# Kernel optimization log

Measured on AMD Instinct MI355X. Metric: run time of the kernel, lower is better.

## Reference

```python
import jax, jax.numpy as jnp
import numpy as np
import math

B, SQ, SKV, D, H, DFF = 8, 256, 1024, 1024, 16, 4096
DK = D // H
EPS = 1e-5


def layer_norm(x, g, b):
    mu = jnp.mean(x, axis=-1, keepdims=True)
    var = jnp.mean((x - mu) ** 2, axis=-1, keepdims=True)
    return (x - mu) * jax.lax.rsqrt(var + EPS) * g + b


def erf_gelu(x):
    return x * 0.5 * (1.0 + jax.lax.erf(x / jnp.sqrt(jnp.float32(2.0))))


def setup_inputs() -> dict:
    key = jax.random.key(0)
    ks = jax.random.split(key, 10)
    s = 0.02
    w = lambda k, shape: jax.random.normal(k, shape, jnp.float32) * s
    return {
        "memory": jax.random.normal(ks[0], (B, SKV, D), jnp.float32),
        "q": jax.random.normal(ks[1], (B, SQ, D), jnp.float32),
        "Wq": w(ks[2], (D, D)), "bq": jnp.zeros((D,), jnp.float32),
        "Wk": w(ks[3], (D, D)), "bk": jnp.zeros((D,), jnp.float32),
        "Wv": w(ks[4], (D, D)), "bv": jnp.zeros((D,), jnp.float32),
        "Wo": w(ks[5], (D, D)), "bo": jnp.zeros((D,), jnp.float32),
        "g_kv": jnp.ones((D,), jnp.float32), "b_kv": jnp.zeros((D,), jnp.float32),
        "g_q": jnp.ones((D,), jnp.float32), "b_q": jnp.zeros((D,), jnp.float32),
        "g_ff": jnp.ones((D,), jnp.float32), "b_ff": jnp.zeros((D,), jnp.float32),
        "W1": w(ks[6], (D, DFF)), "b1": jnp.zeros((DFF,), jnp.float32),
        "W2": w(ks[7], (DFF, D)), "b2": jnp.zeros((D,), jnp.float32),
    }


def reference(memory, q, Wq, bq, Wk, bk, Wv, bv, Wo, bo,
              g_kv, b_kv, g_q, b_q, g_ff, b_ff, W1, b1, W2, b2):
    # Pre-norms
    kv_ = layer_norm(memory, g_kv, b_kv)   # [B, SKV, D]
    q_ = layer_norm(q, g_q, b_q)           # [B, SQ, D]
    # QKV projections, split heads: [B, H, S, DK]
    Q = (q_ @ Wq + bq).reshape(B, SQ, H, DK).transpose(0, 2, 1, 3)
    K = (kv_ @ Wk + bk).reshape(B, SKV, H, DK).transpose(0, 2, 1, 3)
    V = (kv_ @ Wv + bv).reshape(B, SKV, H, DK).transpose(0, 2, 1, 3)
    # Scaled dot-product cross-attention
    scores = jnp.einsum("bhqd,bhkd->bhqk", Q, K) / math.sqrt(DK)
    attn = jax.nn.softmax(scores, axis=-1)  # [B, H, SQ, SKV]
    ctx = jnp.einsum("bhqk,bhkd->bhqd", attn, V)
    ctx = ctx.transpose(0, 2, 1, 3).reshape(B, SQ, D)
    x = ctx @ Wo + bo  # attention output (no residual with q, per source)
    # FeedForwardBlock: x + FFN(LN(x))
    y = layer_norm(x, g_ff, b_ff)
    y = erf_gelu(y @ W1 + b1) @ W2 + b2
    out = y + x
    return (out, attn)
```

## Files before the change

### kernel.cpp

```cpp
#include <hip/hip_runtime.h>
#include <hip/hip_bf16.h>
#include <math.h>

#define B_   8
#define SQ_  256
#define SKV_ 1024
#define D_   1024
#define H_   16
#define DK_  64
#define DFF_ 4096

typedef __attribute__((ext_vector_type(4))) float f32x4;
typedef __attribute__((ext_vector_type(8))) __bf16 bf16x8;

__device__ __forceinline__ unsigned short f2bf(float f) {
    unsigned u = __builtin_bit_cast(unsigned, f);
    u += 0x7FFFu + ((u >> 16) & 1u);
    return (unsigned short)(u >> 16);
}
__device__ __forceinline__ float bf2f(unsigned short h) {
    unsigned u = (unsigned)h << 16;
    return __builtin_bit_cast(float, u);
}

__device__ __forceinline__ void gload_lds16(const void* g, void* l) {
    __builtin_amdgcn_global_load_lds(
        (__attribute__((address_space(1))) void*)g,
        (__attribute__((address_space(3))) void*)l,
        16, 0, 0);
}

__global__ __launch_bounds__(256) void transpose4_k(
    const float* __restrict__ Wa, const float* __restrict__ Wb,
    const float* __restrict__ Wc, const float* __restrict__ Wd,
    unsigned short* __restrict__ Ta, unsigned short* __restrict__ Tb,
    unsigned short* __restrict__ Tc, unsigned short* __restrict__ Td) {
    const float* Ws[4] = {Wa, Wb, Wc, Wd};
    unsigned short* Ts[4] = {Ta, Tb, Tc, Td};
    const float* W = Ws[blockIdx.z];
    unsigned short* Wt = Ts[blockIdx.z];
    __shared__ float t[32][33];
    const int n0 = blockIdx.x * 32, k0 = blockIdx.y * 32;
    const int tx = threadIdx.x, ty = threadIdx.y;
#pragma unroll
    for (int i = ty; i < 32; i += 8)
        t[i][tx] = W[(long)(k0 + i) * 1024 + n0 + tx];
    __syncthreads();
#pragma unroll
    for (int i = ty; i < 32; i += 8)
        Wt[(long)(n0 + i) * 1024 + k0 + tx] = f2bf(t[tx][i]);
}

__global__ __launch_bounds__(256) void transpose_cast_k(
    const float* __restrict__ W, unsigned short* __restrict__ Wt, int K, int N) {
    __shared__ float t[32][33];
    const int n0 = blockIdx.x * 32, k0 = blockIdx.y * 32;
    const int tx = threadIdx.x, ty = threadIdx.y;
#pragma unroll
    for (int i = ty; i < 32; i += 8)
        t[i][tx] = W[(long)(k0 + i) * N + n0 + tx];
    __syncthreads();
#pragma unroll
    for (int i = ty; i < 32; i += 8)
        Wt[(long)(n0 + i) * K + k0 + tx] = f2bf(t[tx][i]);
}

__global__ __launch_bounds__(256) void ln_k(
    const float* __restrict__ x, const float* __restrict__ g,
    const float* __restrict__ b, unsigned short* __restrict__ out) {
    const long row = blockIdx.x;
    const float4* xr = reinterpret_cast<const float4*>(x) + row * 256;
    const int t = threadIdx.x;
    float4 v = xr[t];
    __shared__ float sb[8];

    float s = v.x + v.y + v.z + v.w;
#pragma unroll
    for (int o = 1; o < 64; o <<= 1) s += __shfl_xor(s, o);
    if ((t & 63) == 0) sb[t >> 6] = s;
    __syncthreads();
    const float mu = (sb[0] + sb[1] + sb[2] + sb[3]) * (1.0f / 1024.0f);

    const float dx = v.x - mu, dy = v.y - mu, dz = v.z - mu, dw = v.w - mu;
    float q2 = dx * dx + dy * dy + dz * dz + dw * dw;
#pragma unroll
    for (int o = 1; o < 64; o <<= 1) q2 += __shfl_xor(q2, o);
    if ((t & 63) == 0) sb[4 + (t >> 6)] = q2;
    __syncthreads();
    const float var = (sb[4] + sb[5] + sb[6] + sb[7]) * (1.0f / 1024.0f);
    const float rs = rsqrtf(var + 1e-5f);

    const float4 gv = reinterpret_cast<const float4*>(g)[t];
    const float4 bv = reinterpret_cast<const float4*>(b)[t];
    ushort4 h4;
    h4.x = f2bf(dx * rs * gv.x + bv.x);
    h4.y = f2bf(dy * rs * gv.y + bv.y);
    h4.z = f2bf(dz * rs * gv.z + bv.z);
    h4.w = f2bf(dw * rs * gv.w + bv.w);
    reinterpret_cast<ushort4*>(out)[row * 256 + t] = h4;
}

#define ELD 1032
__global__ __launch_bounds__(512) void fattn_k(
    const unsigned short* __restrict__ Qh,
    const unsigned short* __restrict__ Kh,
    const unsigned short* __restrict__ Vt,
    float* __restrict__ attn,
    unsigned short* __restrict__ ctx) {
    __shared__ unsigned short E_lds[64 * ELD];
    __shared__ unsigned short Q_lds[64 * 64];
    __shared__ unsigned short KV_lds[2][64 * 64];
    __shared__ float partial[8][64];
    __shared__ float invs_l[64];

    const int tid = threadIdx.x;
    const int wid = tid >> 6, lane = tid & 63;
    const int wr = wid >> 2, wc = wid & 3;
    const int r16 = lane & 15, kch = lane >> 4;
    const int z = blockIdx.x, qb = blockIdx.y;
    const int m0 = qb * 64;
    const long qoff = (long)z * (SQ_ * DK_) + (long)m0 * DK_;
    const long koff = (long)z * (SKV_ * DK_);
    const long voff = (long)z * (DK_ * SKV_);

    gload_lds16(Qh + qoff + tid * 8, &Q_lds[wid * 512]);
    gload_lds16(Kh + koff + tid * 8, &KV_lds[0][wid * 512]);
    __syncthreads();

    const f32x4 z4 = {0.f, 0.f, 0.f, 0.f};

    int cur = 0;
    for (int kt = 0; kt < 16; ++kt) {
        if (kt + 1 < 16)
            gload_lds16(Kh + koff + (kt + 1) * (64 * 64) + tid * 8,
                        &KV_lds[cur ^ 1][wid * 512]);
        f32x4 s[2] = {z4, z4};
        const int bro = (wc * 16 + r16) * 64;
#pragma unroll
        for (int k0 = 0; k0 < 64; k0 += 32) {
            const bf16x8 bfrag =
                *reinterpret_cast<const bf16x8*>(&KV_lds[cur][bro + k0 + kch * 8]);
#pragma unroll
            for (int fm = 0; fm < 2; ++fm) {
                const bf16x8 afrag = *reinterpret_cast<const bf16x8*>(
                    &Q_lds[(wr * 32 + fm * 16 + r16) * 64 + k0 + kch * 8]);
                s[fm] = __builtin_amdgcn_mfma_f32_16x16x32_bf16(afrag, bfrag, s[fm], 0, 0, 0);
            }
        }
#pragma unroll
        for (int fm = 0; fm < 2; ++fm)
#pragma unroll
            for (int j = 0; j < 4; ++j) {
                const int row = wr * 32 + fm * 16 + kch * 4 + j;
                const int col = kt * 64 + wc * 16 + r16;
                E_lds[row * ELD + col] = f2bf(__expf(s[fm][j] * 0.125f));
            }
        __syncthreads();
        cur ^= 1;
    }

    {
        const int r = tid & 63, c = tid >> 6;
        float s = 0.f;
        const unsigned* p = reinterpret_cast<const unsigned*>(&E_lds[r * ELD + c * 128]);
#pragma unroll
        for (int i = 0; i < 64; ++i) {
            const unsigned u = p[i];
            s += __builtin_bit_cast(float, u << 16) +
                 __builtin_bit_cast(float, u & 0xffff0000u);
        }
        partial[c][r] = s;
    }
    __syncthreads();
    if (tid < 64) {
        float t = 0.f;
#pragma unroll
        for (int c = 0; c < 8; ++c) t += partial[c][tid];
        invs_l[tid] = 1.0f / t;
    }
    __syncthreads();

    gload_lds16(Vt + voff + (tid >> 3) * SKV_ + (tid & 7) * 8, &KV_lds[0][wid * 512]);

    {
        float* abase = attn + (long)z * (SQ_ * SKV_) + (long)m0 * SKV_;
#pragma unroll
        for (int ro = 0; ro < 8; ++ro) {
            const int row = ro * 8 + wid;
            const float inv = invs_l[row];
#pragma unroll
            for (int cc = 0; cc < 4; ++cc) {
                const int col = cc * 256 + lane * 4;
                const ushort4 e4 =
                    *reinterpret_cast<const ushort4*>(&E_lds[row * ELD + col]);
                float4 o;
                o.x = bf2f(e4.x) * inv; o.y = bf2f(e4.y) * inv;
                o.z = bf2f(e4.z) * inv; o.w = bf2f(e4.w) * inv;
                reinterpret_cast<float4*>(abase + (long)row * SKV_)[col >> 2] = o;
            }
        }
    }
    __syncthreads();

    cur = 0;
    f32x4 acc[2] = {z4, z4};
    for (int kt = 0; kt < 16; ++kt) {
        if (kt + 1 < 16)
            gload_lds16(Vt + voff + (tid >> 3) * SKV_ + (kt + 1) * 64 + (tid & 7) * 8,
                        &KV_lds[cur ^ 1][wid * 512]);
        const int bro = (wc * 16 + r16) * 64;
#pragma unroll
        for (int k0 = 0; k0 < 64; k0 += 32) {
            const bf16x8 bfrag =
                *reinterpret_cast<const bf16x8*>(&KV_lds[cur][bro + k0 + kch * 8]);
#pragma unroll
            for (int fm = 0; fm < 2; ++fm) {
                const bf16x8 afrag = *reinterpret_cast<const bf16x8*>(
                    &E_lds[(wr * 32 + fm * 16 + r16) * ELD + kt * 64 + k0 + kch * 8]);
                acc[fm] = __builtin_amdgcn_mfma_f32_16x16x32_bf16(afrag, bfrag, acc[fm], 0, 0, 0);
            }
        }
        __syncthreads();
        cur ^= 1;
    }

    const int b = z >> 4, h = z & 15;
#pragma unroll
    for (int fm = 0; fm < 2; ++fm)
#pragma unroll
        for (int j = 0; j < 4; ++j) {
            const int row = wr * 32 + fm * 16 + kch * 4 + j;
            const int col = wc * 16 + r16;
            const float v = acc[fm][j] * invs_l[row];
            ctx[((long)(b * SQ_) + m0 + row) * D_ + h * 64 + col] = f2bf(v);
        }
}

__global__ __launch_bounds__(256) void reduce4_k(
    const float* __restrict__ part, const float* __restrict__ bias,
    const float* __restrict__ resid, float* __restrict__ out) {
    const long i4 = (long)blockIdx.x * 256 + threadIdx.x;
    const float4* p = reinterpret_cast<const float4*>(part);
    const float4 a = p[i4], b = p[i4 + 524288], c = p[i4 + 1048576],
                 d = p[i4 + 1572864];
    const float4 bb = reinterpret_cast<const float4*>(bias)[i4 & 255];
    const float4 r = reinterpret_cast<const float4*>(resid)[i4];
    float4 o;
    o.x = a.x + b.x + c.x + d.x + bb.x + r.x;
    o.y = a.y + b.y + c.y + d.y + bb.y + r.y;
    o.z = a.z + b.z + c.z + d.z + bb.z + r.z;
    o.w = a.w + b.w + c.w + d.w + bb.w + r.w;
    reinterpret_cast<float4*>(out)[i4] = o;
}

enum GemmMode {
    M_QSPLIT  = 0,
    M_KVSPLIT = 1,
    M_BIASF   = 2,
    M_GELU    = 3,
    M_PART    = 4
};

template <int BM, int BN, int MODE>
__global__ __launch_bounds__(256, 2) void gemm_k(
    const unsigned short* __restrict__ A,
    const unsigned short* __restrict__ Bt,
    const float* __restrict__ bias,
    const float* __restrict__ bias2,
    float* __restrict__ outF,
    unsigned short* __restrict__ outH,
    int M, int N, int K, int lda, int ldb,
    long sA, long sB, long sC,
    float alpha) {
    constexpr int WM = BM / 2, WN = BN / 2;
    constexpr int FM = WM / 16, FN = WN / 16;
    __shared__ unsigned short ldsA[2][BM * 32];
    __shared__ unsigned short ldsB[2][BN * 32];

    const int tid = threadIdx.x;
    const int wid = tid >> 6, lane = tid & 63;
    const int wr = wid >> 1, wc = wid & 1;
    const int r16 = lane & 15, kch = lane >> 4;
    const int z = blockIdx.z;
    const long zA = (long)z * sA, zB = (long)z * sB;
    const int m0 = blockIdx.y * BM, n0 = blockIdx.x * BN;

    auto stage = [&](int buf, int kt) {
        const int k0 = kt * 32;
#pragma unroll
        for (int j = 0; j < BM / 64; ++j) {
            const int e = (j * 256 + tid) * 8, rr = e >> 5, cc = e & 31;
            gload_lds16(A + zA + (long)(m0 + rr) * lda + (k0 + cc),
                        &ldsA[buf][(j * 256 + wid * 64) * 8]);
        }
#pragma unroll
        for (int j = 0; j < BN / 64; ++j) {
            const int e = (j * 256 + tid) * 8, rr = e >> 5, cc = e & 31;
            gload_lds16(Bt + zB + (long)(n0 + rr) * ldb + (k0 + cc),
                        &ldsB[buf][(j * 256 + wid * 64) * 8]);
        }
    };

    const f32x4 zero4 = {0.f, 0.f, 0.f, 0.f};
    f32x4 acc[FM][FN];
#pragma unroll
    for (int i = 0; i < FM; ++i)
#pragma unroll
        for (int j = 0; j < FN; ++j) acc[i][j] = zero4;

    const int nK = K / 32;
    stage(0, 0);
    __syncthreads();
    int cur = 0;
    for (int kt = 0; kt < nK; ++kt) {
        if (kt + 1 < nK) stage(cur ^ 1, kt + 1);

        bf16x8 af[FM], bfr[FN];
#pragma unroll
        for (int fm = 0; fm < FM; ++fm)
            af[fm] = *reinterpret_cast<const bf16x8*>(
                &ldsA[cur][(wr * WM + fm * 16 + r16) * 32 + kch * 8]);
#pragma unroll
        for (int fn = 0; fn < FN; ++fn)
            bfr[fn] = *reinterpret_cast<const bf16x8*>(
                &ldsB[cur][(wc * WN + fn * 16 + r16) * 32 + kch * 8]);
#pragma unroll
        for (int fm = 0; fm < FM; ++fm)
#pragma unroll
            for (int fn = 0; fn < FN; ++fn)
                acc[fm][fn] = __builtin_amdgcn_mfma_f32_16x16x32_bf16(
                    af[fm], bfr[fn], acc[fm][fn], 0, 0, 0);
        __syncthreads();
        cur ^= 1;
    }

#pragma unroll
    for (int fm = 0; fm < FM; ++fm) {
#pragma unroll
        for (int fn = 0; fn < FN; ++fn) {
            const int gn = n0 + wc * WN + fn * 16 + r16;
            float bv = 0.0f;
            if constexpr (MODE == M_QSPLIT || MODE == M_BIASF || MODE == M_GELU)
                bv = bias[gn];
            if constexpr (MODE == M_KVSPLIT)
                bv = (gn < 1024) ? bias[gn] : bias2[gn - 1024];
#pragma unroll
            for (int j = 0; j < 4; ++j) {
                const int gm = m0 + wr * WM + fm * 16 + kch * 4 + j;
                const float v = acc[fm][fn][j];
                if constexpr (MODE == M_QSPLIT) {
                    const int bb = gm >> 8, ss = gm & 255, hh = gn >> 6, dd = gn & 63;
                    outH[(((long)(bb * H_ + hh)) * SQ_ + ss) * DK_ + dd] = f2bf(v + bv);
                } else if constexpr (MODE == M_KVSPLIT) {
                    const int bb = gm >> 10, ss = gm & 1023;
                    if (gn < 1024) {
                        const int hh = gn >> 6, dd = gn & 63;
                        outH[(((long)(bb * H_ + hh)) * SKV_ + ss) * DK_ + dd] = f2bf(v + bv);
                    } else {
                        const int gv = gn - 1024, hh = gv >> 6, dd = gv & 63;
                        outH[(size_t)8192 * 1024 +
                             (((long)(bb * H_ + hh)) * DK_ + dd) * SKV_ + ss] = f2bf(v + bv);
                    }
                } else if constexpr (MODE == M_BIASF) {
                    outF[(long)gm * N + gn] = v + bv;
                } else if constexpr (MODE == M_GELU) {
                    const float u = v + bv;
                    outH[(long)gm * N + gn] =
                        f2bf(u * 0.5f * (1.0f + erff(u * 0.70710678f)));
                } else {
                    outF[(long)z * sC + (long)gm * N + gn] = v;
                }
            }
        }
    }
    (void)alpha;
}

extern "C" void kernel_launch(void* const* d_in, const int* in_sizes, int n_in,
                              void* d_out, int out_size, void* d_ws, size_t ws_size,
                              hipStream_t stream) {
    (void)in_sizes; (void)n_in; (void)out_size; (void)ws_size;
    const float* memory = (const float*)d_in[0];
    const float* q      = (const float*)d_in[1];
    const float* Wq = (const float*)d_in[2];  const float* bq = (const float*)d_in[3];
    const float* Wk = (const float*)d_in[4];  const float* bk = (const float*)d_in[5];
    const float* Wv = (const float*)d_in[6];  const float* bv = (const float*)d_in[7];
    const float* Wo = (const float*)d_in[8];  const float* bo = (const float*)d_in[9];
    const float* g_kv = (const float*)d_in[10]; const float* b_kv = (const float*)d_in[11];
    const float* g_q  = (const float*)d_in[12]; const float* b_q  = (const float*)d_in[13];
    const float* g_ff = (const float*)d_in[14]; const float* b_ff = (const float*)d_in[15];
    const float* W1 = (const float*)d_in[16]; const float* b1 = (const float*)d_in[17];
    const float* W2 = (const float*)d_in[18]; const float* b2 = (const float*)d_in[19];

    float* outO = (float*)d_out;
    float* outA = outO + (size_t)2048 * 1024;

    char* w = (char*)d_ws;
    unsigned short* kvB  = (unsigned short*)w; w += (size_t)8192 * 1024 * 2;
    unsigned short* qB   = (unsigned short*)w; w += (size_t)2048 * 1024 * 2;
    unsigned short* WqT  = (unsigned short*)w; w += (size_t)1024 * 1024 * 2;
    unsigned short* WkvT = (unsigned short*)w; w += (size_t)2048 * 1024 * 2;
    unsigned short* WoT  = (unsigned short*)w; w += (size_t)1024 * 1024 * 2;
    unsigned short* W1T  = (unsigned short*)w; w += (size_t)4096 * 1024 * 2;
    unsigned short* W2T  = (unsigned short*)w; w += (size_t)1024 * 4096 * 2;
    unsigned short* Qh   = (unsigned short*)w; w += (size_t)2048 * 1024 * 2;
    unsigned short* KVh  = (unsigned short*)w; w += (size_t)16384 * 1024 * 2;
    unsigned short* ctxB = (unsigned short*)w; w += (size_t)2048 * 1024 * 2;
    float*          xF   = (float*)w;          w += (size_t)2048 * 1024 * 4;
    unsigned short* yB   = (unsigned short*)w; w += (size_t)2048 * 1024 * 2;
    unsigned short* h1B  = (unsigned short*)w; w += (size_t)2048 * 4096 * 2;
    float*          part = (float*)w;          w += (size_t)4 * 2048 * 1024 * 4;

    unsigned short* Kh = KVh;
    unsigned short* Vt = KVh + (size_t)8192 * 1024;

    const dim3 blk(256);
    transpose4_k<<<dim3(32, 32, 4), dim3(32, 8), 0, stream>>>(
        Wq, Wk, Wv, Wo, WqT, WkvT, WkvT + (size_t)1024 * 1024, WoT);
    transpose_cast_k<<<dim3(128, 32), dim3(32, 8), 0, stream>>>(W1, W1T, 1024, 4096);
    transpose_cast_k<<<dim3(32, 128), dim3(32, 8), 0, stream>>>(W2, W2T, 4096, 1024);

    ln_k<<<8192, blk, 0, stream>>>(memory, g_kv, b_kv, kvB);
    ln_k<<<2048, blk, 0, stream>>>(q, g_q, b_q, qB);

    gemm_k<64, 128, M_QSPLIT><<<dim3(8, 32, 1), blk, 0, stream>>>(
        qB, WqT, bq, nullptr, nullptr, Qh, 2048, 1024, 1024, 1024, 1024, 0, 0, 0, 1.f);
    gemm_k<128, 128, M_KVSPLIT><<<dim3(16, 64, 1), blk, 0, stream>>>(
        kvB, WkvT, bk, bv, nullptr, KVh, 8192, 2048, 1024, 1024, 1024, 0, 0, 0, 1.f);

    fattn_k<<<dim3(128, 4), dim3(512), 0, stream>>>(Qh, Kh, Vt, outA, ctxB);

    gemm_k<64, 128, M_BIASF><<<dim3(8, 32, 1), blk, 0, stream>>>(
        ctxB, WoT, bo, nullptr, xF, nullptr, 2048, 1024, 1024, 1024, 1024, 0, 0, 0, 1.f);

    ln_k<<<2048, blk, 0, stream>>>(xF, g_ff, b_ff, yB);

    gemm_k<128, 128, M_GELU><<<dim3(32, 16, 1), blk, 0, stream>>>(
        yB, W1T, b1, nullptr, nullptr, h1B, 2048, 4096, 1024, 1024, 1024, 0, 0, 0, 1.f);

    gemm_k<128, 128, M_PART><<<dim3(8, 16, 4), blk, 0, stream>>>(
        h1B, W2T, nullptr, nullptr, part, nullptr, 2048, 1024, 1024, 4096, 4096,
        1024, 1024, (long)2048 * 1024, 1.f);
    reduce4_k<<<2048, blk, 0, stream>>>(part, b2, xF, outO);
}
```

Measured before the change: 499.3 us.

## Add 256x256 tiled GEMM kernel with swizzled LDS for KV, FFN1, FFN2

Adds a new 512-thread GEMM kernel that uses 256x256 output tiles and a K-step of 64. It stages global-to-LDS loads with an XOR swizzle, double-buffers with explicit vmcnt waits, and raises wave priority around the MFMA bursts. The large KV projection and both FFN GEMMs move to this kernel, while the older kernel keeps only the Q and output projections. Bigger tiles raise data reuse per LDS load, but they also mean fewer blocks, roughly 64–256 per launch, and 128 KB of LDS per block, which limits occupancy to one block per CU and risks poor load balance on the smaller launches.

```diff
diff --git a/kernel.cpp b/kernel.cpp
--- a/kernel.cpp
+++ b/kernel.cpp
@@ -261,6 +261,142 @@
     M_PART    = 4
 };
 
+template <int MODE>
+__global__ __launch_bounds__(512, 2) void gemm256_k(
+    const unsigned short* __restrict__ A,
+    const unsigned short* __restrict__ Bt,
+    const float* __restrict__ bias,
+    const float* __restrict__ bias2,
+    float* __restrict__ outF,
+    unsigned short* __restrict__ outH,
+    int M, int N, int K, int lda, int ldb,
+    long sA, long sB, long sC) {
+    __shared__ unsigned short ldsA[2][256 * 64];
+    __shared__ unsigned short ldsB[2][256 * 64];
+
+    const int tid = threadIdx.x;
+    const int wid = tid >> 6, lane = tid & 63;
+    const int wr = wid >> 2, wc = wid & 3;
+    const int r16 = lane & 15, kch = lane >> 4;
+    const int z = blockIdx.z;
+    const long zA = (long)z * sA, zB = (long)z * sB;
+    const int m0 = blockIdx.y * 256, n0 = blockIdx.x * 256;
+
+    auto stage = [&](int p, int kt) {
+        const int k0 = kt * 64;
+#pragma unroll
+        for (int i = 0; i < 4; ++i) {
+            const int pb = (i * 512 + tid) * 16;
+            const int lb = pb ^ (((pb >> 7) & 7) << 4);
+            const int row = lb >> 7, col = (lb & 127) >> 1;
+            gload_lds16(A + zA + (long)(m0 + row) * lda + (k0 + col),
+                        &ldsA[p][(i * 512 + wid * 64) * 8]);
+        }
+#pragma unroll
+        for (int i = 0; i < 4; ++i) {
+            const int pb = (i * 512 + tid) * 16;
+            const int lb = pb ^ (((pb >> 7) & 7) << 4);
+            const int row = lb >> 7, col = (lb & 127) >> 1;
+            gload_lds16(Bt + zB + (long)(n0 + row) * ldb + (k0 + col),
+                        &ldsB[p][(i * 512 + wid * 64) * 8]);
+        }
+    };
+    auto ldA = [&](int p, int row, int kk) {
+        const int lb = row * 128 + kk * 64 + kch * 16;
+        const int pb = lb ^ ((row & 7) << 4);
+        return *reinterpret_cast<const bf16x8*>(
+            reinterpret_cast<const char*>(&ldsA[p][0]) + pb);
+    };
+    auto ldB = [&](int p, int row, int kk) {
+        const int lb = row * 128 + kk * 64 + kch * 16;
+        const int pb = lb ^ ((row & 7) << 4);
+        return *reinterpret_cast<const bf16x8*>(
+            reinterpret_cast<const char*>(&ldsB[p][0]) + pb);
+    };
+
+    f32x4 acc[8][4];
+#pragma unroll
+    for (int i = 0; i < 8; ++i)
+#pragma unroll
+        for (int j = 0; j < 4; ++j) acc[i][j] = {0.f, 0.f, 0.f, 0.f};
+
+    const int nK = K >> 6;
+    stage(0, 0);
+    stage(1, 1);
+
+    for (int kt = 0; kt < nK; ++kt) {
+        const int p = kt & 1;
+        if (kt < nK - 1) asm volatile("s_waitcnt vmcnt(8)" ::: "memory");
+        else             asm volatile("s_waitcnt vmcnt(0)" ::: "memory");
+        __builtin_amdgcn_s_barrier();
+        __builtin_amdgcn_sched_barrier(0);
+
+        bf16x8 bfr[4][2];
+#pragma unroll
+        for (int fn = 0; fn < 4; ++fn) {
+            bfr[fn][0] = ldB(p, wc * 64 + fn * 16 + r16, 0);
+            bfr[fn][1] = ldB(p, wc * 64 + fn * 16 + r16, 1);
+        }
+#pragma unroll
+        for (int q = 0; q < 4; ++q) {
+            bf16x8 af[2][2];
+#pragma unroll
+            for (int i = 0; i < 2; ++i) {
+                af[i][0] = ldA(p, wr * 128 + (2 * q + i) * 16 + r16, 0);
+                af[i][1] = ldA(p, wr * 128 + (2 * q + i) * 16 + r16, 1);
+            }
+            __builtin_amdgcn_s_setprio(1);
+#pragma unroll
+            for (int i = 0; i < 2; ++i)
+#pragma unroll
+                for (int fn = 0; fn < 4; ++fn) {
+                    acc[2 * q + i][fn] = __builtin_amdgcn_mfma_f32_16x16x32_bf16(
+                        af[i][0], bfr[fn][0], acc[2 * q + i][fn], 0, 0, 0);
+                    acc[2 * q + i][fn] = __builtin_amdgcn_mfma_f32_16x16x32_bf16(
+                        af[i][1], bfr[fn][1], acc[2 * q + i][fn], 0, 0, 0);
+                }
+            __builtin_amdgcn_s_setprio(0);
+            __builtin_amdgcn_s_barrier();
+        }
+        __builtin_amdgcn_sched_barrier(0);
+        if (kt + 2 < nK) stage(p, kt + 2);
+    }
+
+#pragma unroll
+    for (int fm = 0; fm < 8; ++fm) {
+#pragma unroll
+        for (int fn = 0; fn < 4; ++fn) {
+            const int gn = n0 + wc * 64 + fn * 16 + r16;
+            float bv = 0.0f;
+            if constexpr (MODE == M_GELU) bv = bias[gn];
+            if constexpr (MODE == M_KVSPLIT)
+                bv = (gn < 1024) ? bias[gn] : bias2[gn - 1024];
+#pragma unroll
+            for (int j = 0; j < 4; ++j) {
+                const int gm = m0 + wr * 128 + fm * 16 + kch * 4 + j;
+                const float v = acc[fm][fn][j];
+                if constexpr (MODE == M_KVSPLIT) {
+                    const int bb = gm >> 10, ss = gm & 1023;
+                    if (gn < 1024) {
+                        const int hh = gn >> 6, dd = gn & 63;
+                        outH[(((long)(bb * H_ + hh)) * SKV_ + ss) * DK_ + dd] = f2bf(v + bv);
+                    } else {
+                        const int gv = gn - 1024, hh = gv >> 6, dd = gv & 63;
+                        outH[(size_t)8192 * 1024 +
+                             (((long)(bb * H_ + hh)) * DK_ + dd) * SKV_ + ss] = f2bf(v + bv);
+                    }
+                } else if constexpr (MODE == M_GELU) {
+                    const float u = v + bv;
+                    outH[(long)gm * N + gn] =
+                        f2bf(u * 0.5f * (1.0f + erff(u * 0.70710678f)));
+                } else {
+                    outF[(long)z * sC + (long)gm * N + gn] = v;
+                }
+            }
+        }
+    }
+}
+
 template <int BM, int BN, int MODE>
 __global__ __launch_bounds__(256, 2) void gemm_k(
     const unsigned short* __restrict__ A,
@@ -340,10 +476,7 @@
         for (int fn = 0; fn < FN; ++fn) {
             const int gn = n0 + wc * WN + fn * 16 + r16;
             float bv = 0.0f;
-            if constexpr (MODE == M_QSPLIT || MODE == M_BIASF || MODE == M_GELU)
-                bv = bias[gn];
-            if constexpr (MODE == M_KVSPLIT)
-                bv = (gn < 1024) ? bias[gn] : bias2[gn - 1024];
+            if constexpr (MODE == M_QSPLIT || MODE == M_BIASF) bv = bias[gn];
 #pragma unroll
             for (int j = 0; j < 4; ++j) {
                 const int gm = m0 + wr * WM + fm * 16 + kch * 4 + j;
@@ -351,29 +484,13 @@
                 if constexpr (MODE == M_QSPLIT) {
                     const int bb = gm >> 8, ss = gm & 255, hh = gn >> 6, dd = gn & 63;
                     outH[(((long)(bb * H_ + hh)) * SQ_ + ss) * DK_ + dd] = f2bf(v + bv);
-                } else if constexpr (MODE == M_KVSPLIT) {
-                    const int bb = gm >> 10, ss = gm & 1023;
-                    if (gn < 1024) {
-                        const int hh = gn >> 6, dd = gn & 63;
-                        outH[(((long)(bb * H_ + hh)) * SKV_ + ss) * DK_ + dd] = f2bf(v + bv);
-                    } else {
-                        const int gv = gn - 1024, hh = gv >> 6, dd = gv & 63;
-                        outH[(size_t)8192 * 1024 +
-                             (((long)(bb * H_ + hh)) * DK_ + dd) * SKV_ + ss] = f2bf(v + bv);
-                    }
                 } else if constexpr (MODE == M_BIASF) {
                     outF[(long)gm * N + gn] = v + bv;
-                } else if constexpr (MODE == M_GELU) {
-                    const float u = v + bv;
-                    outH[(long)gm * N + gn] =
-                        f2bf(u * 0.5f * (1.0f + erff(u * 0.70710678f)));
-                } else {
-                    outF[(long)z * sC + (long)gm * N + gn] = v;
                 }
             }
         }
     }
-    (void)alpha;
+    (void)alpha; (void)bias2;
 }
 
 extern "C" void kernel_launch(void* const* d_in, const int* in_sizes, int n_in,
@@ -425,8 +542,8 @@
 
     gemm_k<64, 128, M_QSPLIT><<<dim3(8, 32, 1), blk, 0, stream>>>(
         qB, WqT, bq, nullptr, nullptr, Qh, 2048, 1024, 1024, 1024, 1024, 0, 0, 0, 1.f);
-    gemm_k<128, 128, M_KVSPLIT><<<dim3(16, 64, 1), blk, 0, stream>>>(
-        kvB, WkvT, bk, bv, nullptr, KVh, 8192, 2048, 1024, 1024, 1024, 0, 0, 0, 1.f);
+    gemm256_k<M_KVSPLIT><<<dim3(8, 32, 1), dim3(512), 0, stream>>>(
+        kvB, WkvT, bk, bv, nullptr, KVh, 8192, 2048, 1024, 1024, 1024, 0, 0, 0);
 
     fattn_k<<<dim3(128, 4), dim3(512), 0, stream>>>(Qh, Kh, Vt, outA, ctxB);
 
@@ -435,11 +552,11 @@
 
     ln_k<<<2048, blk, 0, stream>>>(xF, g_ff, b_ff, yB);
 
-    gemm_k<128, 128, M_GELU><<<dim3(32, 16, 1), blk, 0, stream>>>(
-        yB, W1T, b1, nullptr, nullptr, h1B, 2048, 4096, 1024, 1024, 1024, 0, 0, 0, 1.f);
-
-    gemm_k<128, 128, M_PART><<<dim3(8, 16, 4), blk, 0, stream>>>(
+    gemm256_k<M_GELU><<<dim3(16, 8, 1), dim3(512), 0, stream>>>(
+        yB, W1T, b1, nullptr, nullptr, h1B, 2048, 4096, 1024, 1024, 1024, 0, 0, 0);
+
+    gemm256_k<M_PART><<<dim3(4, 8, 4), dim3(512), 0, stream>>>(
         h1B, W2T, nullptr, nullptr, part, nullptr, 2048, 1024, 1024, 4096, 4096,
-        1024, 1024, (long)2048 * 1024, 1.f);
+        1024, 1024, (long)2048 * 1024);
     reduce4_k<<<2048, blk, 0, stream>>>(part, b2, xF, outO);
 }
```

Result: slower. 529.0 us (+5.9%).
